# Kernel tuning notes

Measured on AMD Instinct MI355X. Metric: run time of the kernel, lower is better.

Reference implementation:

```python
import jax, jax.numpy as jnp
import numpy as np

GROUPS = 32  # min(32, 256//4)
EPS = 1e-5


def setup_inputs() -> dict:
    key = jax.random.key(0)
    ks = jax.random.split(key, 4)
    B, C, H, W = 8, 256, 128, 128
    x = jax.random.normal(ks[0], (B, C, H, W), dtype=jnp.float32)
    gn_w = jnp.ones((C,), dtype=jnp.float32)
    gn_b = jnp.zeros((C,), dtype=jnp.float32)
    qkv_w = jax.random.normal(ks[1], (3 * C, C), dtype=jnp.float32) * (C ** -0.5)
    qkv_b = jnp.zeros((3 * C,), dtype=jnp.float32)
    proj_w = jax.random.normal(ks[2], (C, C), dtype=jnp.float32) * (C ** -0.5)
    proj_b = jnp.zeros((C,), dtype=jnp.float32)
    return {"x": x, "gn_w": gn_w, "gn_b": gn_b, "qkv_w": qkv_w,
            "qkv_b": qkv_b, "proj_w": proj_w, "proj_b": proj_b}


def _group_norm(x, w, b):
    B, C, H, W = x.shape
    xg = x.reshape(B, GROUPS, C // GROUPS, H, W)
    mean = xg.mean(axis=(2, 3, 4), keepdims=True)
    var = xg.var(axis=(2, 3, 4), keepdims=True)
    xg = (xg - mean) * jax.lax.rsqrt(var + EPS)
    x = xg.reshape(B, C, H, W)
    return x * w[None, :, None, None] + b[None, :, None, None]


def reference(x, gn_w, gn_b, qkv_w, qkv_b, proj_w, proj_b):
    B, C, H, W = x.shape
    num_heads = 8
    head_dim = C // num_heads
    scale = head_dim ** -0.5

    h = _group_norm(x, gn_w, gn_b)
    # 1x1 conv == per-pixel matmul over channels
    qkv = jnp.einsum('bchw,oc->bohw', h, qkv_w) + qkv_b[None, :, None, None]
    qkv = qkv.reshape(B, 3, num_heads, head_dim, H * W)
    q, k, v = qkv[:, 0], qkv[:, 1], qkv[:, 2]  # each (B, h, head_dim, HW)
    # Faithful to source: contracts over spatial axis d=HW -> (B,h,hd,hd)
    attn = jnp.einsum('bhid,bhjd->bhij', q, k) * scale
    attn = jax.nn.softmax(attn, axis=-1)
    out = jnp.einsum('bhij,bhjd->bhid', attn, v)  # (B, h, head_dim, HW)
    out = out.reshape(B, C, H, W)
    out = jnp.einsum('bchw,oc->bohw', out, proj_w) + proj_b[None, :, None, None]
    return x + out
```

## Files before the change

kernel.cpp:

```cpp
#include <hip/hip_runtime.h>
#include <stdint.h>

typedef __bf16 bf16;
typedef __attribute__((ext_vector_type(8))) __bf16 bf16x8;
typedef __attribute__((ext_vector_type(4))) float f32x4;

#define S_HW 16384
#define N_C 256

__device__ __forceinline__ f32x4 mfma16(bf16x8 a, bf16x8 b, f32x4 c) {
  return __builtin_amdgcn_mfma_f32_16x16x32_bf16(a, b, c, 0, 0, 0);
}
__device__ __forceinline__ void async_ld16(const bf16* g, bf16* l) {
  __builtin_amdgcn_global_load_lds(
      (const __attribute__((address_space(1))) unsigned int*)g,
      (__attribute__((address_space(3))) unsigned int*)l, 16, 0, 0);
}
__device__ __forceinline__ unsigned short bf2u(bf16 h) {
  union { bf16 h; unsigned short u; } c; c.h = h; return c.u;
}
__device__ __forceinline__ bf16 u2bf(unsigned short u) {
  union { unsigned short u; bf16 h; } c; c.u = u; return c.h;
}

__global__ __launch_bounds__(256) void k_split(
    const float* __restrict__ x, bf16* __restrict__ yhi, bf16* __restrict__ ylo,
    bf16* __restrict__ yt, float* __restrict__ Sx) {
  int b = blockIdx.z, c0 = blockIdx.y * 64, s0 = blockIdx.x * 64;
  __shared__ unsigned T[64][65];
  __shared__ float sxl[256];
  int t = threadIdx.x;
  int cl = t >> 2, sg = t & 3;
  size_t off = (size_t)(b * N_C + c0 + cl) * S_HW + s0 + sg * 16;
  const float* xp = x + off;
  bf16x8 hv[2], lv[2];
  float sum = 0.f;
#pragma unroll
  for (int i2 = 0; i2 < 4; i2++) {
    float4 v = *(const float4*)(xp + i2 * 4);
    float f4[4] = {v.x, v.y, v.z, v.w};
#pragma unroll
    for (int k = 0; k < 4; k++) {
      int i = i2 * 4 + k;
      float fv = f4[k];
      bf16 h = (bf16)fv;
      bf16 l = (bf16)(fv - (float)h);
      hv[i >> 3][i & 7] = h;
      lv[i >> 3][i & 7] = l;
      sum += fv;
      T[sg * 16 + i][cl] = (unsigned)bf2u(h) | ((unsigned)bf2u(l) << 16);
    }
  }
  *(bf16x8*)(yhi + off) = hv[0];
  *(bf16x8*)(yhi + off + 8) = hv[1];
  *(bf16x8*)(ylo + off) = lv[0];
  *(bf16x8*)(ylo + off + 8) = lv[1];
  sxl[t] = sum;
  __syncthreads();
  if (t < 64) {
    float s2 = sxl[t * 4] + sxl[t * 4 + 1] + sxl[t * 4 + 2] + sxl[t * 4 + 3];
    atomicAdd(&Sx[b * N_C + c0 + t], s2);
  }
  int sl = t >> 2, cg = t & 3;
  bf16x8 ho[2], lo2[2];
#pragma unroll
  for (int i = 0; i < 16; i++) {
    unsigned u = T[sl][cg * 16 + i];
    ho[i >> 3][i & 7] = u2bf((unsigned short)(u & 0xffffu));
    lo2[i >> 3][i & 7] = u2bf((unsigned short)(u >> 16));
  }
  size_t tb = (size_t)(b * S_HW + s0 + sl) * 512 + c0 + cg * 16;
  *(bf16x8*)(yt + tb) = ho[0];
  *(bf16x8*)(yt + tb + 8) = ho[1];
  *(bf16x8*)(yt + tb + 256) = lo2[0];
  *(bf16x8*)(yt + tb + 256 + 8) = lo2[1];
}

__global__ __launch_bounds__(256) void k_gram(
    const bf16* __restrict__ yhi, const bf16* __restrict__ ylo,
    float* __restrict__ YG3) {
  constexpr int BK = 32;
  constexpr int NT = 64;
  constexpr int BUF = 128 * BK;
  __shared__ __align__(16) bf16 As[3 * BUF];
  __shared__ __align__(16) bf16 Bs[3 * BUF];
  int kc = blockIdx.x * 2048;
  int m0 = (blockIdx.y >> 2) * 128, n0 = (blockIdx.y & 3) * 128;
  int b = blockIdx.z;
  int tid = threadIdx.x, lane = tid & 63, wave = tid >> 6;
  int wm = (wave >> 1) * 64, wn = (wave & 1) * 64;
  const bf16* Ab = yhi + (size_t)(b * N_C + m0) * S_HW;
  const bf16* Bb = (n0 < 256) ? yhi + (size_t)(b * N_C + n0) * S_HW
                              : ylo + (size_t)(b * N_C + n0 - 256) * S_HW;
  f32x4 acc[4][4] = {};
  int fm = lane & 15, fk = (lane >> 4) * 8;

  auto STAGE = [&](int bi, int t) {
    int kt = kc + t * BK;
#pragma unroll
    for (int i = 0; i < 2; i++) {
      int ch = i * 256 + tid;
      int row = ch >> 2, col = (ch & 3) * 8;
      async_ld16(Ab + (size_t)row * S_HW + kt + col,
                 As + bi * BUF + (i * 256 + wave * 64) * 8);
      async_ld16(Bb + (size_t)row * S_HW + kt + col,
                 Bs + bi * BUF + (i * 256 + wave * 64) * 8);
    }
  };

  STAGE(0, 0);
  STAGE(1, 1);
  STAGE(2, 2);
  int bi = 0;
  for (int t = 0; t < NT - 2; t++) {
    asm volatile("s_waitcnt vmcnt(8)" ::: "memory");
    __builtin_amdgcn_s_barrier();
    const bf16* Ap = As + bi * BUF;
    const bf16* Bp = Bs + bi * BUF;
    bf16x8 af[4], bfr[4];
#pragma unroll
    for (int q = 0; q < 4; q++) {
      af[q] = *(const bf16x8*)(Ap + (wm + q * 16 + fm) * BK + fk);
      bfr[q] = *(const bf16x8*)(Bp + (wn + q * 16 + fm) * BK + fk);
    }
    asm volatile("s_waitcnt lgkmcnt(0)" ::: "memory");
    __builtin_amdgcn_sched_barrier(0);
    __builtin_amdgcn_s_barrier();
    if (t + 3 < NT) STAGE(bi, t + 3);
#pragma unroll
    for (int ti = 0; ti < 4; ti++)
#pragma unroll
      for (int tj = 0; tj < 4; tj++)
        acc[ti][tj] = mfma16(af[ti], bfr[tj], acc[ti][tj]);
    bi = (bi == 2) ? 0 : bi + 1;
  }
#pragma unroll
  for (int pe = 0; pe < 2; pe++) {
    if (pe == 0)
      asm volatile("s_waitcnt vmcnt(4)" ::: "memory");
    else
      asm volatile("s_waitcnt vmcnt(0)" ::: "memory");
    __builtin_amdgcn_s_barrier();
    const bf16* Ap = As + bi * BUF;
    const bf16* Bp = Bs + bi * BUF;
    bf16x8 af[4], bfr[4];
#pragma unroll
    for (int q = 0; q < 4; q++) {
      af[q] = *(const bf16x8*)(Ap + (wm + q * 16 + fm) * BK + fk);
      bfr[q] = *(const bf16x8*)(Bp + (wn + q * 16 + fm) * BK + fk);
    }
#pragma unroll
    for (int ti = 0; ti < 4; ti++)
#pragma unroll
      for (int tj = 0; tj < 4; tj++)
        acc[ti][tj] = mfma16(af[ti], bfr[tj], acc[ti][tj]);
    bi = (bi == 2) ? 0 : bi + 1;
  }
  int quad = lane >> 4, cn = lane & 15;
#pragma unroll
  for (int ti = 0; ti < 4; ti++)
#pragma unroll
    for (int r = 0; r < 4; r++) {
      int m = m0 + wm + ti * 16 + quad * 4 + r;
#pragma unroll
      for (int tj = 0; tj < 4; tj++) {
        int n = n0 + wn + tj * 16 + cn;
        atomicAdd(&YG3[(size_t)(b * N_C + m) * 512 + n], acc[ti][tj][r]);
      }
    }
}

__global__ __launch_bounds__(256) void k_wkt(const float* __restrict__ qkv_w,
                                             float* __restrict__ WkT) {
  int k = blockIdx.x, j = threadIdx.x;
  WkT[k * 256 + j] = qkv_w[(256 + j) * 256 + k];
}

__global__ __launch_bounds__(256) void k_coefs(
    const float* __restrict__ Sx, const float* __restrict__ YG3,
    const float* __restrict__ gn_w, const float* __restrict__ gn_b,
    const float* __restrict__ qkv_w, const float* __restrict__ qkv_b,
    float* __restrict__ a_, float* __restrict__ bv_, float* __restrict__ u_,
    float* __restrict__ vbe) {
  int b = blockIdx.x, role = blockIdx.y, t = threadIdx.x;
  __shared__ float sxl[256], gxd[256], gm[32], gr[32], sh[256], bl[256];
  __shared__ float ured[64][4];
  sxl[t] = Sx[b * N_C + t];
  gxd[t] = YG3[(size_t)(b * N_C + t) * 512 + t] +
           2.f * YG3[(size_t)(b * N_C + t) * 512 + 256 + t];
  __syncthreads();
  if (t < 32) {
    float s = 0.f, q2 = 0.f;
#pragma unroll
    for (int i = 0; i < 8; i++) { s += sxl[t * 8 + i]; q2 += gxd[t * 8 + i]; }
    float mean = s * (1.f / 131072.f);
    float var = q2 * (1.f / 131072.f) - mean * mean;
    gm[t] = mean;
    gr[t] = 1.f / sqrtf(var + 1e-5f);
  }
  __syncthreads();
  {
    float A = gn_w[t] * gr[t >> 3];
    float B = gn_b[t] - gm[t >> 3] * A;
    bl[t] = B;
    sh[t] = A * sxl[t] + 16384.f * B;
    if (role == 0) {
      a_[b * N_C + t] = A;
      bv_[b * N_C + t] = B;
    }
  }
  __syncthreads();
  if (role == 0) {
    const float* wp = qkv_w + (size_t)(512 + t) * 256;
    float acc = 0.f;
    for (int c = 0; c < 256; c++) acc += wp[c] * bl[c];
    vbe[b * N_C + t] = acc + qkv_b[512 + t];
  } else {
    int r = (role - 1) * 64 + (t >> 2);
    int seg = (t & 3) * 64;
    const float* wp = qkv_w + (size_t)r * 256 + seg;
    float p = 0.f;
    for (int c = 0; c < 64; c++) p += wp[c] * sh[seg + c];
    ured[t >> 2][t & 3] = p;
    __syncthreads();
    if (t < 64)
      u_[b * 512 + (role - 1) * 64 + t] =
          ured[t][0] + ured[t][1] + ured[t][2] + ured[t][3];
  }
}

__global__ __launch_bounds__(256) void k_t1(
    const float* __restrict__ YG3, const float* __restrict__ WkT,
    const float* __restrict__ a_, const float* __restrict__ bv_,
    const float* __restrict__ Sx, float* __restrict__ T1) {
  int tile = blockIdx.x, b = blockIdx.y;
  int i0 = (tile >> 2) * 64, j0 = (tile & 3) * 64;
  __shared__ float As[64][69];
  __shared__ float Bs[64][69];
  __shared__ float al[256], bl[256], sxl[256];
  int t = threadIdx.x;
  al[t] = a_[b * N_C + t];
  bl[t] = bv_[b * N_C + t];
  sxl[t] = Sx[b * N_C + t];
  int cl = t >> 2, qq = (t & 3) * 16;
  int kk = t >> 2, jj = (t & 3) * 16;
  int ti = t >> 4, tj = t & 15;
  float acc[4][4] = {};
  for (int kc = 0; kc < 256; kc += 64) {
    {
      const float* yg = YG3 + (size_t)(b * N_C + i0 + cl) * 512 + kc + qq;
#pragma unroll
      for (int i = 0; i < 16; i++) As[cl][qq + i] = yg[i] + yg[256 + i];
    }
    __syncthreads();
    {
      int cp = kc + kk;
      const float* ygp = YG3 + (size_t)(b * N_C + cp) * 512 + 256 + i0 + jj;
#pragma unroll
      for (int i = 0; i < 16; i++) As[jj + i][kk] += ygp[i];
    }
    __syncthreads();
    {
      int c = i0 + cl;
      float ac = al[c], bc = bl[c], sxc = sxl[c];
#pragma unroll
      for (int i = 0; i < 16; i++) {
        int cp = kc + qq + i;
        As[cl][qq + i] = ac * al[cp] * As[cl][qq + i] + ac * bl[cp] * sxc +
                         bc * al[cp] * sxl[cp] + 16384.f * bc * bl[cp];
      }
    }
    {
      const float* wp = WkT + (size_t)(kc + kk) * 256 + j0 + jj;
#pragma unroll
      for (int i = 0; i < 16; i += 4) {
        float4 v = *(const float4*)(wp + i);
        Bs[kk][jj + i] = v.x; Bs[kk][jj + i + 1] = v.y;
        Bs[kk][jj + i + 2] = v.z; Bs[kk][jj + i + 3] = v.w;
      }
    }
    __syncthreads();
    for (int k = 0; k < 64; k++) {
      float av[4], bv4[4];
#pragma unroll
      for (int ii = 0; ii < 4; ii++) av[ii] = As[ti * 4 + ii][k];
#pragma unroll
      for (int j2 = 0; j2 < 4; j2++) bv4[j2] = Bs[k][tj * 4 + j2];
#pragma unroll
      for (int ii = 0; ii < 4; ii++)
#pragma unroll
        for (int j2 = 0; j2 < 4; j2++) acc[ii][j2] += av[ii] * bv4[j2];
    }
    __syncthreads();
  }
#pragma unroll
  for (int ii = 0; ii < 4; ii++)
#pragma unroll
    for (int j2 = 0; j2 < 4; j2++)
      T1[(size_t)(b * N_C + i0 + ti * 4 + ii) * 256 + j0 + tj * 4 + j2] =
          acc[ii][j2];
}

__global__ __launch_bounds__(256) void k_logits(
    const float* __restrict__ T1, const float* __restrict__ qkv_w,
    const float* __restrict__ qkv_b, const float* __restrict__ u_,
    float* __restrict__ attn) {
  int h = blockIdx.x, b = blockIdx.y;
  __shared__ float Tc[64][33];
  __shared__ float Wql[32][65];
  __shared__ float Ll[32][33];
  __shared__ float uq[32], uk[32], bq[32], bk[32];
  int t = threadIdx.x;
  if (t < 32) {
    uq[t] = u_[b * 512 + h * 32 + t];
    uk[t] = u_[b * 512 + 256 + h * 32 + t];
    bq[t] = qkv_b[h * 32 + t];
    bk[t] = qkv_b[256 + h * 32 + t];
  }
  int i = t & 31, jg = t >> 5;
  float acc[4] = {};
  for (int cc = 0; cc < 256; cc += 64) {
    {
      int c_l = t >> 2, seg = (t & 3) * 8;
      const float* tp = T1 + (size_t)(b * N_C + cc + c_l) * 256 + h * 32 + seg;
      float4 v0 = *(const float4*)tp, v1 = *(const float4*)(tp + 4);
      Tc[c_l][seg] = v0.x; Tc[c_l][seg + 1] = v0.y;
      Tc[c_l][seg + 2] = v0.z; Tc[c_l][seg + 3] = v0.w;
      Tc[c_l][seg + 4] = v1.x; Tc[c_l][seg + 5] = v1.y;
      Tc[c_l][seg + 6] = v1.z; Tc[c_l][seg + 7] = v1.w;
      int row = t >> 3, seg2 = (t & 7) * 8;
      const float* wp = qkv_w + (size_t)(h * 32 + row) * 256 + cc + seg2;
      float4 w0 = *(const float4*)wp, w1 = *(const float4*)(wp + 4);
      Wql[row][seg2] = w0.x; Wql[row][seg2 + 1] = w0.y;
      Wql[row][seg2 + 2] = w0.z; Wql[row][seg2 + 3] = w0.w;
      Wql[row][seg2 + 4] = w1.x; Wql[row][seg2 + 5] = w1.y;
      Wql[row][seg2 + 6] = w1.z; Wql[row][seg2 + 7] = w1.w;
    }
    __syncthreads();
    for (int c = 0; c < 64; c++) {
      float w = Wql[i][c];
#pragma unroll
      for (int j2 = 0; j2 < 4; j2++) acc[j2] += w * Tc[c][jg * 4 + j2];
    }
    __syncthreads();
  }
  const float scale = 0.17677669529663687f;
#pragma unroll
  for (int j2 = 0; j2 < 4; j2++) {
    int j = jg * 4 + j2;
    Ll[i][j] = scale * (acc[j2] + bq[i] * uk[j] + bk[j] * uq[i] +
                        16384.f * bq[i] * bk[j]);
  }
  __syncthreads();
  if (t < 32) {
    float m = -1e30f;
    for (int j = 0; j < 32; j++) m = fmaxf(m, Ll[t][j]);
    float e[32], s = 0.f;
    for (int j = 0; j < 32; j++) { e[j] = expf(Ll[t][j] - m); s += e[j]; }
    float inv = 1.f / s;
    float* ap = attn + (size_t)((b * 8 + h) * 32 + t) * 32;
    for (int j = 0; j < 32; j++) ap[j] = e[j] * inv;
  }
}

__global__ __launch_bounds__(256) void k_pv(
    const float* __restrict__ proj_w, const float* __restrict__ attn,
    const float* __restrict__ qkv_w, const float* __restrict__ a_,
    const float* __restrict__ vbe, const float* __restrict__ proj_b,
    bf16* __restrict__ FA, float* __restrict__ g_) {
  int tile = blockIdx.x, b = blockIdx.y;
  int i0 = (tile >> 2) * 64, j0 = (tile & 3) * 64;
  __shared__ float As[64][69];
  __shared__ float Bs[64][69];
  __shared__ float At[2][32][33];
  __shared__ float gred[64][4];
  int t = threadIdx.x;
  int cl = t >> 2, qq = (t & 3) * 16;
  int kk = t >> 2, jj = (t & 3) * 16;
  int ti = t >> 4, tj = t & 15;
  float acc[4][4] = {};
  float gacc = 0.f;
  for (int kc = 0; kc < 256; kc += 64) {
    int h0 = kc >> 5;
    __syncthreads();
    {
      const float* ap = attn + (size_t)b * 8192 + h0 * 1024;
#pragma unroll
      for (int i = 0; i < 8; i++) {
        int idx = t * 8 + i;
        At[idx >> 10][(idx >> 5) & 31][idx & 31] = ap[idx];
      }
      const float* wp = qkv_w + (size_t)(512 + kc + kk) * 256 + j0 + jj;
#pragma unroll
      for (int i = 0; i < 16; i += 4) {
        float4 v = *(const float4*)(wp + i);
        Bs[kk][jj + i] = v.x; Bs[kk][jj + i + 1] = v.y;
        Bs[kk][jj + i + 2] = v.z; Bs[kk][jj + i + 3] = v.w;
      }
    }
    __syncthreads();
    {
      int hl = qq >> 5;
      int jbase = qq & 31;
      const float* pp = proj_w + (size_t)(i0 + cl) * 256 + (h0 + hl) * 32;
      float pr[32];
#pragma unroll
      for (int i = 0; i < 32; i += 4) {
        float4 v = *(const float4*)(pp + i);
        pr[i] = v.x; pr[i + 1] = v.y; pr[i + 2] = v.z; pr[i + 3] = v.w;
      }
#pragma unroll
      for (int i = 0; i < 16; i++) {
        int jm = jbase + i;
        float s = 0.f;
#pragma unroll
        for (int ii = 0; ii < 32; ii++) s += pr[ii] * At[hl][ii][jm];
        As[cl][qq + i] = s;
        gacc += s * vbe[b * N_C + kc + qq + i];
      }
    }
    __syncthreads();
    for (int k = 0; k < 64; k++) {
      float av[4], bv4[4];
#pragma unroll
      for (int ii = 0; ii < 4; ii++) av[ii] = As[ti * 4 + ii][k];
#pragma unroll
      for (int j2 = 0; j2 < 4; j2++) bv4[j2] = Bs[k][tj * 4 + j2];
#pragma unroll
      for (int ii = 0; ii < 4; ii++)
#pragma unroll
        for (int j2 = 0; j2 < 4; j2++) acc[ii][j2] += av[ii] * bv4[j2];
    }
  }
  __syncthreads();
  gred[cl][t & 3] = gacc;
  __syncthreads();
  if ((tile & 3) == 0 && t < 64)
    g_[b * N_C + i0 + t] =
        gred[t][0] + gred[t][1] + gred[t][2] + gred[t][3] + proj_b[i0 + t];
  float a4[4];
  {
    float4 v = *(const float4*)(a_ + b * N_C + j0 + tj * 4);
    a4[0] = v.x; a4[1] = v.y; a4[2] = v.z; a4[3] = v.w;
  }
#pragma unroll
  for (int ii = 0; ii < 4; ii++) {
    int row = i0 + ti * 4 + ii;
#pragma unroll
    for (int j2 = 0; j2 < 4; j2++) {
      int col = j0 + tj * 4 + j2;
      float f = acc[ii][j2] * a4[j2] + (row == col ? 1.0f : 0.0f);
      bf16 hi = (bf16)f;
      bf16 lo = (bf16)(f - (float)hi);
      FA[(size_t)(b * N_C + row) * 512 + col] = hi;
      FA[(size_t)(b * N_C + row) * 512 + 256 + col] = lo;
    }
  }
}

__global__ __launch_bounds__(256) void k_final(
    const bf16* __restrict__ FA, const bf16* __restrict__ yt,
    const float* __restrict__ g_, float* __restrict__ out) {
  constexpr int BK = 32;
  constexpr int NT = 24;
  constexpr int BUF = 128 * BK;
  __shared__ __align__(16) bf16 As[3 * BUF];
  __shared__ __align__(16) bf16 Bs[3 * BUF];
  int b = blockIdx.z, m0 = blockIdx.y * 128, n0 = blockIdx.x * 128;
  int tid = threadIdx.x, lane = tid & 63, wave = tid >> 6;
  int wm = (wave >> 1) * 64, wn = (wave & 1) * 64;
  const bf16* Ab = FA + (size_t)(b * N_C + m0) * 512;
  const bf16* Bb = yt + (size_t)(b * S_HW + n0) * 512;
  f32x4 acc[4][4] = {};
  int fm = lane & 15, fk = (lane >> 4) * 8;

  auto STAGE = [&](int bi, int t) {
    int kt = t * BK;
    int ka = (kt < 512) ? kt : kt - 512;
    int kb = (kt < 256) ? kt : kt - 256;
#pragma unroll
    for (int i = 0; i < 2; i++) {
      int ch = i * 256 + tid;
      int row = ch >> 2, col = (ch & 3) * 8;
      async_ld16(Ab + (size_t)row * 512 + ka + col,
                 As + bi * BUF + (i * 256 + wave * 64) * 8);
      async_ld16(Bb + (size_t)row * 512 + kb + col,
                 Bs + bi * BUF + (i * 256 + wave * 64) * 8);
    }
  };

  STAGE(0, 0);
  STAGE(1, 1);
  STAGE(2, 2);
  int bi = 0;
  for (int t = 0; t < NT - 2; t++) {
    asm volatile("s_waitcnt vmcnt(8)" ::: "memory");
    __builtin_amdgcn_s_barrier();
    const bf16* Ap = As + bi * BUF;
    const bf16* Bp = Bs + bi * BUF;
    bf16x8 af[4], bfr[4];
#pragma unroll
    for (int q = 0; q < 4; q++) {
      af[q] = *(const bf16x8*)(Ap + (wm + q * 16 + fm) * BK + fk);
      bfr[q] = *(const bf16x8*)(Bp + (wn + q * 16 + fm) * BK + fk);
    }
    asm volatile("s_waitcnt lgkmcnt(0)" ::: "memory");
    __builtin_amdgcn_sched_barrier(0);
    __builtin_amdgcn_s_barrier();
    if (t + 3 < NT) STAGE(bi, t + 3);
#pragma unroll
    for (int ti = 0; ti < 4; ti++)
#pragma unroll
      for (int tj = 0; tj < 4; tj++)
        acc[ti][tj] = mfma16(af[ti], bfr[tj], acc[ti][tj]);
    bi = (bi == 2) ? 0 : bi + 1;
  }
#pragma unroll
  for (int pe = 0; pe < 2; pe++) {
    if (pe == 0)
      asm volatile("s_waitcnt vmcnt(4)" ::: "memory");
    else
      asm volatile("s_waitcnt vmcnt(0)" ::: "memory");
    __builtin_amdgcn_s_barrier();
    const bf16* Ap = As + bi * BUF;
    const bf16* Bp = Bs + bi * BUF;
    bf16x8 af[4], bfr[4];
#pragma unroll
    for (int q = 0; q < 4; q++) {
      af[q] = *(const bf16x8*)(Ap + (wm + q * 16 + fm) * BK + fk);
      bfr[q] = *(const bf16x8*)(Bp + (wn + q * 16 + fm) * BK + fk);
    }
#pragma unroll
    for (int ti = 0; ti < 4; ti++)
#pragma unroll
      for (int tj = 0; tj < 4; tj++)
        acc[ti][tj] = mfma16(af[ti], bfr[tj], acc[ti][tj]);
    bi = (bi == 2) ? 0 : bi + 1;
  }
  int quad = lane >> 4, cn = lane & 15;
#pragma unroll
  for (int ti = 0; ti < 4; ti++)
#pragma unroll
    for (int r = 0; r < 4; r++) {
      int row = m0 + wm + ti * 16 + quad * 4 + r;
      float gb = g_[b * N_C + row];
#pragma unroll
      for (int tj = 0; tj < 4; tj++) {
        int col = n0 + wn + tj * 16 + cn;
        size_t idx = (size_t)(b * N_C + row) * S_HW + col;
        out[idx] = acc[ti][tj][r] + gb;
      }
    }
}

extern "C" void kernel_launch(void* const* d_in, const int* in_sizes, int n_in,
                              void* d_out, int out_size, void* d_ws,
                              size_t ws_size, hipStream_t stream) {
  const float* x = (const float*)d_in[0];
  const float* gn_w = (const float*)d_in[1];
  const float* gn_b = (const float*)d_in[2];
  const float* qkv_w = (const float*)d_in[3];
  const float* qkv_b = (const float*)d_in[4];
  const float* proj_w = (const float*)d_in[5];
  const float* proj_b = (const float*)d_in[6];
  float* out = (float*)d_out;

  const size_t MB = 1ull << 20;
  char* ws = (char*)d_ws;
  bf16* ylo = (bf16*)ws;
  bf16* yt = (bf16*)(ws + 64 * MB);
  float* YG3 = (float*)(ws + 192 * MB);
  bf16* FA = (bf16*)(ws + 194 * MB);
  float* WkT = (float*)(ws + 196 * MB);
  float* attn = (float*)(ws + 196 * MB + 256 * 1024);
  float* Sx = (float*)(ws + 196 * MB + 512 * 1024);
  float* a_ = (float*)(ws + 196 * MB + 520 * 1024);
  float* bv_ = (float*)(ws + 196 * MB + 528 * 1024);
  float* u_ = (float*)(ws + 196 * MB + 536 * 1024);
  float* vbe = (float*)(ws + 196 * MB + 552 * 1024);
  float* g_ = (float*)(ws + 196 * MB + 560 * 1024);
  float* T1 = (float*)(ws + 198 * MB);
  bf16* yhi = (bf16*)d_out;

  if (ws_size < 200 * MB) return;

  hipMemsetAsync(YG3, 0, 4 * MB + 520 * 1024, stream);
  k_split<<<dim3(256, 4, 8), 256, 0, stream>>>(x, yhi, ylo, yt, Sx);
  k_gram<<<dim3(8, 8, 8), 256, 0, stream>>>(yhi, ylo, YG3);
  k_wkt<<<256, 256, 0, stream>>>(qkv_w, WkT);
  k_coefs<<<dim3(8, 9), 256, 0, stream>>>(Sx, YG3, gn_w, gn_b, qkv_w, qkv_b,
                                          a_, bv_, u_, vbe);
  k_t1<<<dim3(16, 8), 256, 0, stream>>>(YG3, WkT, a_, bv_, Sx, T1);
  k_logits<<<dim3(8, 8), 256, 0, stream>>>(T1, qkv_w, qkv_b, u_, attn);
  k_pv<<<dim3(16, 8), 256, 0, stream>>>(proj_w, attn, qkv_w, a_, vbe, proj_b,
                                        FA, g_);
  k_final<<<dim3(128, 2, 8), 256, 0, stream>>>(FA, yt, g_, out);
}
```

Before: 538.8 us.

## Enlarge k_final tile to full 256 rows with 512 threads, BK=64 and XOR-swizzled LDS

The final GEMM kernel now has each 512-thread block cover all 256 output channels for a 128-pixel column tile. This halves the grid, so each yt B tile is loaded from global memory once instead of twice. The K step is doubled to 64, halving the number of barrier iterations, and an XOR swizzle on the 16-byte chunks in LDS is meant to avoid bank conflicts on fragment reads. The cost is more LDS per block (144KB across three buffers), which lowers occupancy, and more registers per thread for the doubled fragments.

```diff
diff --git a/kernel.cpp b/kernel.cpp
--- a/kernel.cpp
+++ b/kernel.cpp
@@ -458,34 +458,42 @@
   }
 }
 
-__global__ __launch_bounds__(256) void k_final(
+__global__ __launch_bounds__(512) void k_final(
     const bf16* __restrict__ FA, const bf16* __restrict__ yt,
     const float* __restrict__ g_, float* __restrict__ out) {
-  constexpr int BK = 32;
-  constexpr int NT = 24;
-  constexpr int BUF = 128 * BK;
-  __shared__ __align__(16) bf16 As[3 * BUF];
-  __shared__ __align__(16) bf16 Bs[3 * BUF];
-  int b = blockIdx.z, m0 = blockIdx.y * 128, n0 = blockIdx.x * 128;
+  constexpr int BK = 64;
+  constexpr int NT = 12;
+  constexpr int BUFA = 256 * BK;
+  constexpr int BUFB = 128 * BK;
+  __shared__ __align__(16) bf16 As[3 * BUFA];
+  __shared__ __align__(16) bf16 Bs[3 * BUFB];
+  int b = blockIdx.z, n0 = blockIdx.x * 128;
   int tid = threadIdx.x, lane = tid & 63, wave = tid >> 6;
   int wm = (wave >> 1) * 64, wn = (wave & 1) * 64;
-  const bf16* Ab = FA + (size_t)(b * N_C + m0) * 512;
+  const bf16* Ab = FA + (size_t)b * N_C * 512;
   const bf16* Bb = yt + (size_t)(b * S_HW + n0) * 512;
   f32x4 acc[4][4] = {};
-  int fm = lane & 15, fk = (lane >> 4) * 8;
+  int fm = lane & 15, cs = lane >> 4;
 
   auto STAGE = [&](int bi, int t) {
     int kt = t * BK;
     int ka = (kt < 512) ? kt : kt - 512;
     int kb = (kt < 256) ? kt : kt - 256;
 #pragma unroll
+    for (int i = 0; i < 4; i++) {
+      int ch = i * 512 + tid;
+      int row = ch >> 3, slot = ch & 7;
+      int gcol = (slot ^ (row & 7)) * 8;
+      async_ld16(Ab + (size_t)row * 512 + ka + gcol,
+                 As + bi * BUFA + ch * 8);
+    }
+#pragma unroll
     for (int i = 0; i < 2; i++) {
-      int ch = i * 256 + tid;
-      int row = ch >> 2, col = (ch & 3) * 8;
-      async_ld16(Ab + (size_t)row * 512 + ka + col,
-                 As + bi * BUF + (i * 256 + wave * 64) * 8);
-      async_ld16(Bb + (size_t)row * 512 + kb + col,
-                 Bs + bi * BUF + (i * 256 + wave * 64) * 8);
+      int ch = i * 512 + tid;
+      int row = ch >> 3, slot = ch & 7;
+      int gcol = (slot ^ (row & 7)) * 8;
+      async_ld16(Bb + (size_t)row * 512 + kb + gcol,
+                 Bs + bi * BUFB + ch * 8);
     }
   };
 
@@ -494,47 +502,66 @@
   STAGE(2, 2);
   int bi = 0;
   for (int t = 0; t < NT - 2; t++) {
-    asm volatile("s_waitcnt vmcnt(8)" ::: "memory");
+    asm volatile("s_waitcnt vmcnt(12)" ::: "memory");
     __builtin_amdgcn_s_barrier();
-    const bf16* Ap = As + bi * BUF;
-    const bf16* Bp = Bs + bi * BUF;
-    bf16x8 af[4], bfr[4];
+    const bf16* Ap = As + bi * BUFA;
+    const bf16* Bp = Bs + bi * BUFB;
+    bf16x8 af[4][2], bfr[4][2];
 #pragma unroll
     for (int q = 0; q < 4; q++) {
-      af[q] = *(const bf16x8*)(Ap + (wm + q * 16 + fm) * BK + fk);
-      bfr[q] = *(const bf16x8*)(Bp + (wn + q * 16 + fm) * BK + fk);
+      int ra = wm + q * 16 + fm;
+      int rb = wn + q * 16 + fm;
+#pragma unroll
+      for (int h = 0; h < 2; h++) {
+        af[q][h] = *(const bf16x8*)(Ap + ra * BK +
+                                    (((h << 2) | cs) ^ (ra & 7)) * 8);
+        bfr[q][h] = *(const bf16x8*)(Bp + rb * BK +
+                                     (((h << 2) | cs) ^ (rb & 7)) * 8);
+      }
     }
     asm volatile("s_waitcnt lgkmcnt(0)" ::: "memory");
     __builtin_amdgcn_sched_barrier(0);
     __builtin_amdgcn_s_barrier();
     if (t + 3 < NT) STAGE(bi, t + 3);
+    __builtin_amdgcn_sched_barrier(0);
 #pragma unroll
     for (int ti = 0; ti < 4; ti++)
 #pragma unroll
-      for (int tj = 0; tj < 4; tj++)
-        acc[ti][tj] = mfma16(af[ti], bfr[tj], acc[ti][tj]);
+      for (int tj = 0; tj < 4; tj++) {
+        acc[ti][tj] = mfma16(af[ti][0], bfr[tj][0], acc[ti][tj]);
+        acc[ti][tj] = mfma16(af[ti][1], bfr[tj][1], acc[ti][tj]);
+      }
     bi = (bi == 2) ? 0 : bi + 1;
   }
 #pragma unroll
   for (int pe = 0; pe < 2; pe++) {
     if (pe == 0)
-      asm volatile("s_waitcnt vmcnt(4)" ::: "memory");
+      asm volatile("s_waitcnt vmcnt(6)" ::: "memory");
     else
       asm volatile("s_waitcnt vmcnt(0)" ::: "memory");
     __builtin_amdgcn_s_barrier();
-    const bf16* Ap = As + bi * BUF;
-    const bf16* Bp = Bs + bi * BUF;
-    bf16x8 af[4], bfr[4];
+    const bf16* Ap = As + bi * BUFA;
+    const bf16* Bp = Bs + bi * BUFB;
+    bf16x8 af[4][2], bfr[4][2];
 #pragma unroll
     for (int q = 0; q < 4; q++) {
-      af[q] = *(const bf16x8*)(Ap + (wm + q * 16 + fm) * BK + fk);
-      bfr[q] = *(const bf16x8*)(Bp + (wn + q * 16 + fm) * BK + fk);
+      int ra = wm + q * 16 + fm;
+      int rb = wn + q * 16 + fm;
+#pragma unroll
+      for (int h = 0; h < 2; h++) {
+        af[q][h] = *(const bf16x8*)(Ap + ra * BK +
+                                    (((h << 2) | cs) ^ (ra & 7)) * 8);
+        bfr[q][h] = *(const bf16x8*)(Bp + rb * BK +
+                                     (((h << 2) | cs) ^ (rb & 7)) * 8);
+      }
     }
 #pragma unroll
     for (int ti = 0; ti < 4; ti++)
 #pragma unroll
-      for (int tj = 0; tj < 4; tj++)
-        acc[ti][tj] = mfma16(af[ti], bfr[tj], acc[ti][tj]);
+      for (int tj = 0; tj < 4; tj++) {
+        acc[ti][tj] = mfma16(af[ti][0], bfr[tj][0], acc[ti][tj]);
+        acc[ti][tj] = mfma16(af[ti][1], bfr[tj][1], acc[ti][tj]);
+      }
     bi = (bi == 2) ? 0 : bi + 1;
   }
   int quad = lane >> 4, cn = lane & 15;
@@ -542,7 +569,7 @@
   for (int ti = 0; ti < 4; ti++)
 #pragma unroll
     for (int r = 0; r < 4; r++) {
-      int row = m0 + wm + ti * 16 + quad * 4 + r;
+      int row = wm + ti * 16 + quad * 4 + r;
       float gb = g_[b * N_C + row];
 #pragma unroll
       for (int tj = 0; tj < 4; tj++) {
@@ -594,5 +621,5 @@
   k_logits<<<dim3(8, 8), 256, 0, stream>>>(T1, qkv_w, qkv_b, u_, attn);
   k_pv<<<dim3(16, 8), 256, 0, stream>>>(proj_w, attn, qkv_w, a_, vbe, proj_b,
                                         FA, g_);
-  k_final<<<dim3(128, 2, 8), 256, 0, stream>>>(FA, yt, g_, out);
-}
+  k_final<<<dim3(128, 1, 8), 512, 0, stream>>>(FA, yt, g_, out);
+}
```

Result: faster. 520.9 us (-3.3%).
